# Kernel optimization log

Hardware: AMD Instinct MI355X
Metric: run time of the kernel (lower is better)

The kernel has to match this reference:

```python
import jax, jax.numpy as jnp
import numpy as np

D_MODEL = 1024
N_HEADS = 16
D_K = D_MODEL // N_HEADS
NEG_INF = -1.0e9


def setup_inputs() -> dict:
    key = jax.random.key(0)
    ks = jax.random.split(key, 12)
    B, S = 2, 2048
    inp = {
        "q": jax.random.normal(ks[0], (B, S, D_MODEL), dtype=jnp.float32),
        "k": jax.random.normal(ks[1], (B, S, D_MODEL), dtype=jnp.float32),
        "v": jax.random.normal(ks[2], (B, S, D_MODEL), dtype=jnp.float32),
        "mask": jax.random.randint(ks[3], (B, 1, S, S), 0, 2, dtype=jnp.int32),
        "Wq": jax.random.normal(ks[4], (D_MODEL, D_MODEL), dtype=jnp.float32) / np.sqrt(D_MODEL),
        "bq": jnp.zeros((D_MODEL,), dtype=jnp.float32),
        "Wk": jax.random.normal(ks[5], (D_MODEL, D_MODEL), dtype=jnp.float32) / np.sqrt(D_MODEL),
        "bk": jnp.zeros((D_MODEL,), dtype=jnp.float32),
        "Wv": jax.random.normal(ks[6], (D_MODEL, D_MODEL), dtype=jnp.float32) / np.sqrt(D_MODEL),
        "bv": jnp.zeros((D_MODEL,), dtype=jnp.float32),
        "Wo": jax.random.normal(ks[7], (D_MODEL, D_MODEL), dtype=jnp.float32) / np.sqrt(D_MODEL),
        "bo": jnp.zeros((D_MODEL,), dtype=jnp.float32),
    }
    return inp


def _split_heads(x):
    B, S, _ = x.shape
    return x.reshape(B, S, N_HEADS, D_K).transpose(0, 2, 1, 3)  # [B,H,S,Dk]


def reference(q, k, v, mask, Wq, bq, Wk, bk, Wv, bv, Wo, bo):
    # QKV projections (nn.Linear: x @ W.T + b; here W stored as [in,out]-agnostic square)
    query = _split_heads(q @ Wq + bq)
    key_ = _split_heads(k @ Wk + bk)
    value = _split_heads(v @ Wv + bv)

    scale = 1.0 / np.sqrt(D_K).astype(np.float32)
    scores = jnp.einsum("bhqd,bhkd->bhqk", query, key_) * scale  # [B,H,S,S]
    scores = jnp.where(mask == 0, NEG_INF, scores)
    attn = jax.nn.softmax(scores, axis=-1)  # dropout is identity in eval (p=0.0)
    ctx = jnp.einsum("bhqk,bhkd->bhqd", attn, value)  # [B,H,S,Dk]

    B, H, S, Dk = ctx.shape
    ctx = ctx.transpose(0, 2, 1, 3).reshape(B, S, H * Dk)
    return ctx @ Wo + bo
```

## Files before the change

### kernel.cpp

```cpp
#include <hip/hip_runtime.h>
#include <hip/hip_bf16.h>

typedef __bf16 bf16_t;
typedef __bf16 bf16x2 __attribute__((ext_vector_type(2)));
typedef __bf16 bf16x8 __attribute__((ext_vector_type(8)));
typedef float f32x4 __attribute__((ext_vector_type(4)));
typedef float f32x16 __attribute__((ext_vector_type(16)));
typedef unsigned int u32;
typedef unsigned long long u64;

#define S_LEN 2048
#define DM 1024
#define NH 16
#define DK 64
#define M_ROWS 4096
#define SCALE_LOG2E 0.1803368801111204f

__device__ __forceinline__ int sw_off(int row, int col) {
  return row * 64 + ((((col >> 3) ^ row) & 7) << 3) + (col & 7);
}

__device__ __forceinline__ bf16x8 cvt8(const float4& a, const float4& b) {
  bf16x8 v;
  v[0] = (__bf16)a.x; v[1] = (__bf16)a.y; v[2] = (__bf16)a.z; v[3] = (__bf16)a.w;
  v[4] = (__bf16)b.x; v[5] = (__bf16)b.y; v[6] = (__bf16)b.z; v[7] = (__bf16)b.w;
  return v;
}

__device__ __forceinline__ void glds16(const bf16_t* g, bf16_t* l) {
  __builtin_amdgcn_global_load_lds(
      (const __attribute__((address_space(1))) void*)g,
      (__attribute__((address_space(3))) void*)l, 16, 0, 0);
}

__device__ __forceinline__ u32 sbit(u32 m, int c) {
#if __has_builtin(__builtin_amdgcn_sbfe)
  return (u32)__builtin_amdgcn_sbfe((int)m, c, 1);
#else
  return (u32)(((int)(m << (31 - c))) >> 31);
#endif
}
__device__ __forceinline__ float mand(float p, u32 e) {
  return __builtin_bit_cast(float, __builtin_bit_cast(u32, p) & e);
}
__device__ __forceinline__ u32 pack2(float lo, float hi) {
#if __has_builtin(__builtin_amdgcn_cvt_pk_bf16_f32)
  bf16x2 r = __builtin_amdgcn_cvt_pk_bf16_f32(lo, hi);
  return __builtin_bit_cast(u32, r);
#else
  union { __bf16 h[2]; u32 u; } x;
  x.h[0] = (__bf16)lo; x.h[1] = (__bf16)hi;
  return x.u;
#endif
}

union U4B { uint4 u; bf16x8 v; };

__global__ __launch_bounds__(256) void pack_maskT(
    const int* __restrict__ mask, u64* __restrict__ mbT)
{
  const int g = blockIdx.x * 256 + threadIdx.x;
  const int key4 = (g & 511) * 4;
  const int qw = (g >> 9) & 31;
  const int b = g >> 14;
  const int* src = &mask[((size_t)b * S_LEN + qw * 64) * S_LEN + key4];
  u64 b0 = 0, b1 = 0, b2 = 0, b3 = 0;
  #pragma unroll 8
  for (int i = 0; i < 64; ++i) {
    const int4 v = *(const int4*)&src[(size_t)i * S_LEN];
    b0 |= (u64)(v.x != 0) << i;
    b1 |= (u64)(v.y != 0) << i;
    b2 |= (u64)(v.z != 0) << i;
    b3 |= (u64)(v.w != 0) << i;
  }
  u64* dst = &mbT[((size_t)b * 32 + qw) * S_LEN + key4];
  dst[0] = b0; dst[1] = b1; dst[2] = b2; dst[3] = b3;
}

__global__ __launch_bounds__(256) void cvt_inputs(
    const float* __restrict__ q, const float* __restrict__ k,
    const float* __restrict__ v, bf16_t* __restrict__ Xb)
{
  const int z = blockIdx.y;
  const float* __restrict__ src = (z == 0) ? q : ((z == 1) ? k : v);
  const size_t idx = ((size_t)blockIdx.x * 256 + threadIdx.x) * 8;
  const float4 a = *(const float4*)&src[idx];
  const float4 b = *(const float4*)&src[idx + 4];
  *(bf16x8*)&Xb[(size_t)z * M_ROWS * DM + idx] = cvt8(a, b);
}

__global__ __launch_bounds__(256) void transw_kernel(
    const float* __restrict__ Wq, const float* __restrict__ Wk,
    const float* __restrict__ Wv, const float* __restrict__ Wo,
    bf16_t* __restrict__ Wt)
{
  const int z = blockIdx.z;
  const float* __restrict__ W = (z == 0) ? Wq : ((z == 1) ? Wk : ((z == 2) ? Wv : Wo));
  bf16_t* __restrict__ out = Wt + (size_t)z * DM * DM;
  __shared__ float tile[64][65];
  const int tx = threadIdx.x & 31, ty = threadIdx.x >> 5;
  const int k0 = blockIdx.x * 64, n0 = blockIdx.y * 64;
  #pragma unroll
  for (int j = 0; j < 8; ++j) {
    const float2 v = *(const float2*)&W[(size_t)(k0 + ty + 8 * j) * DM + n0 + tx * 2];
    tile[ty + 8 * j][tx * 2] = v.x;
    tile[ty + 8 * j][tx * 2 + 1] = v.y;
  }
  __syncthreads();
  #pragma unroll
  for (int j = 0; j < 8; ++j) {
    const int a = ty + 8 * j;
    bf16x2 p;
    p[0] = (__bf16)tile[tx * 2][a];
    p[1] = (__bf16)tile[tx * 2 + 1][a];
    *(bf16x2*)&out[(size_t)(n0 + a) * DM + k0 + tx * 2] = p;
  }
}

__device__ __forceinline__ void gemm_core(
    const bf16_t* __restrict__ A, const bf16_t* __restrict__ Bt,
    f32x4 (&acc)[4][4])
{
  __shared__ __align__(16) bf16_t As[128 * 32];
  __shared__ __align__(16) bf16_t Bs[128 * 32];
  const int t = threadIdx.x, w = t >> 6, L = t & 63, quad = L >> 4, l16 = L & 15;
  const int m0 = blockIdx.x * 128, n0 = blockIdx.y * 128;
  const int mb = 64 * (w & 1), nb = 64 * (w >> 1);
  const int rowS = t >> 2, subS = (t & 3) * 8;

  for (int k0 = 0; k0 < DM; k0 += 32) {
    __syncthreads();
    glds16(&A[(size_t)(m0 + rowS) * DM + k0 + subS],       &As[t * 8]);
    glds16(&A[(size_t)(m0 + 64 + rowS) * DM + k0 + subS],  &As[2048 + t * 8]);
    glds16(&Bt[(size_t)(n0 + rowS) * DM + k0 + subS],      &Bs[t * 8]);
    glds16(&Bt[(size_t)(n0 + 64 + rowS) * DM + k0 + subS], &Bs[2048 + t * 8]);
    __syncthreads();
    bf16x8 af[4], bfr[4];
    #pragma unroll
    for (int mt = 0; mt < 4; ++mt)
      af[mt] = *(const bf16x8*)&As[(mb + 16 * mt + l16) * 32 + quad * 8];
    #pragma unroll
    for (int ct = 0; ct < 4; ++ct)
      bfr[ct] = *(const bf16x8*)&Bs[(nb + 16 * ct + l16) * 32 + quad * 8];
    #pragma unroll
    for (int mt = 0; mt < 4; ++mt)
      #pragma unroll
      for (int ct = 0; ct < 4; ++ct)
        acc[mt][ct] = __builtin_amdgcn_mfma_f32_16x16x32_bf16(af[mt], bfr[ct], acc[mt][ct], 0, 0, 0);
  }
}

__global__ __launch_bounds__(256) void gemm_qkv(
    const bf16_t* __restrict__ Xb, const bf16_t* __restrict__ Wt,
    const float* __restrict__ bq, const float* __restrict__ bk,
    const float* __restrict__ bv,
    bf16_t* __restrict__ Qp, bf16_t* __restrict__ Ksw, bf16_t* __restrict__ Vpl)
{
  const int z = blockIdx.z;
  const float* __restrict__ bias = (z == 0) ? bq : ((z == 1) ? bk : bv);
  f32x4 acc[4][4] = {};
  gemm_core(Xb + (size_t)z * M_ROWS * DM, Wt + (size_t)z * DM * DM, acc);

  const int t = threadIdx.x, w = t >> 6, L = t & 63, quad = L >> 4, l16 = L & 15;
  const int m0 = blockIdx.x * 128, n0 = blockIdx.y * 128;
  const int mb = 64 * (w & 1), nb = 64 * (w >> 1);
  #pragma unroll
  for (int mt = 0; mt < 4; ++mt)
    #pragma unroll
    for (int ct = 0; ct < 4; ++ct)
      #pragma unroll
      for (int r = 0; r < 4; ++r) {
        const int row = m0 + mb + 16 * mt + quad * 4 + r;
        const int n = n0 + nb + 16 * ct + l16;
        float val = acc[mt][ct][r] + bias[n];
        if (z == 0) {
          Qp[(size_t)row * DM + n] = (__bf16)(val * SCALE_LOG2E);
        } else if (z == 2) {
          Vpl[(size_t)row * DM + n] = (__bf16)val;
        } else {
          const int b_ = row >> 11, s = row & 2047, h = n >> 6, d = n & 63;
          const int bh = b_ * NH + h;
          Ksw[((size_t)bh * 32 + (s >> 6)) * 4096 + sw_off(s & 63, d)] = (__bf16)val;
        }
      }
}

__global__ __launch_bounds__(256) void transpV(
    const bf16_t* __restrict__ Vpl, bf16_t* __restrict__ Vt_sw)
{
  __shared__ bf16_t Tr[64 * 72];
  const int t = threadIdx.x;
  const int key0 = blockIdx.x * 64;
  const int bh = blockIdx.y, b = bh >> 4, h = bh & 15;
  const int r = t >> 2, c = (t & 3) * 16;
  const bf16_t* src = &Vpl[(size_t)(b * S_LEN + key0 + r) * DM + h * DK + c];
  const bf16x8 v0 = *(const bf16x8*)src;
  const bf16x8 v1 = *(const bf16x8*)(src + 8);
  #pragma unroll
  for (int j = 0; j < 8; ++j) {
    Tr[r * 72 + c + j] = v0[j];
    Tr[r * 72 + c + 8 + j] = v1[j];
  }
  __syncthreads();
  const int dv = t >> 2, kc = (t & 3) * 16;
  bf16_t ov[16];
  #pragma unroll
  for (int j = 0; j < 16; ++j) ov[j] = Tr[(kc + j) * 72 + dv];
  bf16_t* dst = &Vt_sw[((size_t)bh * 32 + blockIdx.x) * 4096];
  *(bf16x8*)&dst[sw_off(dv, kc)]     = *(bf16x8*)&ov[0];
  *(bf16x8*)&dst[sw_off(dv, kc + 8)] = *(bf16x8*)&ov[8];
}

__global__ __launch_bounds__(256, 2) void attn_kernel(
    const bf16_t* __restrict__ Qp, const bf16_t* __restrict__ Ksw,
    const bf16_t* __restrict__ Vt_sw, const u64* __restrict__ mbT,
    bf16_t* __restrict__ ctx)
{
  __shared__ __align__(16) bf16_t KV[4 * 4096];
  __shared__ __align__(16) u32 Pd[64 * 68];

  const int t = threadIdx.x;
  const int w = t >> 6, L = t & 63;
  const int wq = w & 1, wk = w >> 1;
  const int l31 = L & 31, h5 = L >> 5;
  const int q0 = blockIdx.x * 128;
  const int bh = blockIdx.y, b = bh >> 4, h = bh & 15;

  bf16_t* K0 = KV;            bf16_t* K1 = KV + 4096;
  bf16_t* V0 = KV + 8192;     bf16_t* V1 = KV + 12288;

  const bf16_t* KbaseG = Ksw + (size_t)bh * 32 * 4096;
  const bf16_t* VbaseG = Vt_sw + (size_t)bh * 32 * 4096;

  bf16x8 qf[2][4];
  #pragma unroll
  for (int mt = 0; mt < 2; ++mt) {
    const bf16_t* qr = &Qp[((size_t)(b * S_LEN) + q0 + 64 * wq + 32 * mt + l31) * DM + h * DK + 8 * h5];
    #pragma unroll
    for (int ks = 0; ks < 4; ++ks) qf[mt][ks] = *(const bf16x8*)&qr[16 * ks];
  }

  bf16x8 ones;
  #pragma unroll
  for (int j = 0; j < 8; ++j) ones[j] = (__bf16)1.0f;

  const int qw = 2 * blockIdx.x + wq;
  const size_t mrow = ((size_t)b * 32 + qw) * S_LEN;
  const u32 sel = (l31 & 1) ? 0x07060302u : 0x05040100u;

  f32x16 O[2][2] = {};
  f32x16 Lacc[2] = {};

  glds16(KbaseG + t * 8, K0 + t * 8);
  glds16(KbaseG + 2048 + t * 8, K0 + 2048 + t * 8);
  glds16(VbaseG + t * 8, V0 + t * 8);
  glds16(VbaseG + 2048 + t * 8, V0 + 2048 + t * 8);

  auto iter = [&](int kt, bf16_t* Kc, bf16_t* Vc, bf16_t* Kn, bf16_t* Vn) {
    __syncthreads();
    const u64 mq = mbT[mrow + (size_t)kt * 64 + 32 * wk + l31];
    if (kt + 1 < 32) {
      const bf16_t* kg = KbaseG + (size_t)(kt + 1) * 4096;
      const bf16_t* vg = VbaseG + (size_t)(kt + 1) * 4096;
      glds16(kg + t * 8, Kn + t * 8);
      glds16(kg + 2048 + t * 8, Kn + 2048 + t * 8);
      glds16(vg + t * 8, Vn + t * 8);
      glds16(vg + 2048 + t * 8, Vn + 2048 + t * 8);
    }

    f32x16 sv[2] = {};
    #pragma unroll
    for (int ks = 0; ks < 4; ++ks) {
      const int ch = ((2 * ks + h5) ^ l31) & 7;
      const bf16x8 kb = *(const bf16x8*)&Kc[(32 * wk + l31) * 64 + ch * 8];
      sv[0] = __builtin_amdgcn_mfma_f32_32x32x16_bf16(qf[0][ks], kb, sv[0], 0, 0, 0);
      sv[1] = __builtin_amdgcn_mfma_f32_32x32x16_bf16(qf[1][ks], kb, sv[1], 0, 0, 0);
    }

    const u32 mlo = (u32)mq, mhi = (u32)(mq >> 32);
    #pragma unroll
    for (int mt = 0; mt < 2; ++mt) {
      const u32 mm = mt ? mhi : mlo;
      #pragma unroll
      for (int rp = 0; rp < 16; rp += 2) {
        const int c = (rp & 3) + 8 * (rp >> 2) + 4 * h5;
        const int p = 32 * wq + 16 * mt + (c >> 1);
        const float p0 = mand(__builtin_exp2f(sv[mt][rp]),     sbit(mm, c));
        const float p1 = mand(__builtin_exp2f(sv[mt][rp + 1]), sbit(mm, c + 1));
        Pd[p * 68 + 32 * wk + l31] = pack2(p0, p1);
      }
    }

    #pragma unroll
    for (int ks = 0; ks < 2; ++ks) {
      bf16x8 pa[2];
      #pragma unroll
      for (int mt = 0; mt < 2; ++mt) {
        const int p = 32 * wq + 16 * mt + (l31 >> 1);
        const int off = p * 68 + 32 * wk + 16 * ks + 8 * h5;
        const uint4 lo = *(const uint4*)&Pd[off];
        const uint4 hi = *(const uint4*)&Pd[off + 4];
        U4B af;
        af.u.x = __builtin_amdgcn_perm(lo.y, lo.x, sel);
        af.u.y = __builtin_amdgcn_perm(lo.w, lo.z, sel);
        af.u.z = __builtin_amdgcn_perm(hi.y, hi.x, sel);
        af.u.w = __builtin_amdgcn_perm(hi.w, hi.z, sel);
        pa[mt] = af.v;
      }
      #pragma unroll
      for (int dvt = 0; dvt < 2; ++dvt) {
        const int ch = ((4 * wk + 2 * ks + h5) ^ l31) & 7;
        const bf16x8 vb = *(const bf16x8*)&Vc[(32 * dvt + l31) * 64 + ch * 8];
        O[0][dvt] = __builtin_amdgcn_mfma_f32_32x32x16_bf16(pa[0], vb, O[0][dvt], 0, 0, 0);
        O[1][dvt] = __builtin_amdgcn_mfma_f32_32x32x16_bf16(pa[1], vb, O[1][dvt], 0, 0, 0);
      }
      Lacc[0] = __builtin_amdgcn_mfma_f32_32x32x16_bf16(pa[0], ones, Lacc[0], 0, 0, 0);
      Lacc[1] = __builtin_amdgcn_mfma_f32_32x32x16_bf16(pa[1], ones, Lacc[1], 0, 0, 0);
    }
  };

  for (int kt = 0; kt < 32; kt += 2) {
    iter(kt,     K0, V0, K1, V1);
    iter(kt + 1, K1, V1, K0, V0);
  }

  __syncthreads();
  float* Osh = (float*)KV;
  float* Lsh = (float*)Pd;
  if (wk == 0) {
    #pragma unroll
    for (int mt = 0; mt < 2; ++mt)
      #pragma unroll
      for (int r = 0; r < 16; ++r) {
        const int ql = 64 * wq + 32 * mt + (r & 3) + 8 * (r >> 2) + 4 * h5;
        Osh[ql * 64 + l31]      = O[mt][0][r];
        Osh[ql * 64 + 32 + l31] = O[mt][1][r];
        if (l31 == 0) Lsh[ql] = Lacc[mt][r];
      }
  }
  __syncthreads();
  if (wk == 1) {
    #pragma unroll
    for (int mt = 0; mt < 2; ++mt)
      #pragma unroll
      for (int r = 0; r < 16; ++r) {
        const int ql = 64 * wq + 32 * mt + (r & 3) + 8 * (r >> 2) + 4 * h5;
        const float inv = 1.0f / (Lacc[mt][r] + Lsh[ql]);
        const size_t obase = ((size_t)(b * S_LEN) + q0 + ql) * DM + h * DK;
        ctx[obase + l31]      = (__bf16)((O[mt][0][r] + Osh[ql * 64 + l31]) * inv);
        ctx[obase + 32 + l31] = (__bf16)((O[mt][1][r] + Osh[ql * 64 + 32 + l31]) * inv);
      }
  }
}

__global__ __launch_bounds__(256) void gemm_out(
    const bf16_t* __restrict__ ctx, const bf16_t* __restrict__ Wto,
    const float* __restrict__ bo, float* __restrict__ out)
{
  f32x4 acc[4][4] = {};
  gemm_core(ctx, Wto, acc);
  const int t = threadIdx.x, w = t >> 6, L = t & 63, quad = L >> 4, l16 = L & 15;
  const int m0 = blockIdx.x * 128, n0 = blockIdx.y * 128;
  const int mb = 64 * (w & 1), nb = 64 * (w >> 1);
  #pragma unroll
  for (int mt = 0; mt < 4; ++mt)
    #pragma unroll
    for (int ct = 0; ct < 4; ++ct)
      #pragma unroll
      for (int r = 0; r < 4; ++r) {
        const int row = m0 + mb + 16 * mt + quad * 4 + r;
        const int n = n0 + nb + 16 * ct + l16;
        out[(size_t)row * DM + n] = acc[mt][ct][r] + bo[n];
      }
}

extern "C" void kernel_launch(void* const* d_in, const int* in_sizes, int n_in,
                              void* d_out, int out_size, void* d_ws, size_t ws_size,
                              hipStream_t stream) {
  const float* q  = (const float*)d_in[0];
  const float* k  = (const float*)d_in[1];
  const float* v  = (const float*)d_in[2];
  const int* mask = (const int*)d_in[3];
  const float* Wq = (const float*)d_in[4];
  const float* bq = (const float*)d_in[5];
  const float* Wk = (const float*)d_in[6];
  const float* bk = (const float*)d_in[7];
  const float* Wv = (const float*)d_in[8];
  const float* bv = (const float*)d_in[9];
  const float* Wo = (const float*)d_in[10];
  const float* bo = (const float*)d_in[11];
  float* out = (float*)d_out;

  const size_t SLICE = (size_t)M_ROWS * DM;
  bf16_t* ws_b = (bf16_t*)d_ws;
  bf16_t* Xb    = ws_b;
  bf16_t* Qp    = ws_b + 3 * SLICE;
  bf16_t* Ksw   = ws_b + 4 * SLICE;
  bf16_t* Vpl   = ws_b + 5 * SLICE;
  bf16_t* Wt    = ws_b + 6 * SLICE;
  u64* mbT      = (u64*)(ws_b + 7 * SLICE);
  bf16_t* Vt_sw = ws_b + 2 * SLICE;
  bf16_t* ctx   = ws_b;

  pack_maskT<<<dim3(128), dim3(256), 0, stream>>>(mask, mbT);
  cvt_inputs<<<dim3(2048, 3), dim3(256), 0, stream>>>(q, k, v, Xb);
  transw_kernel<<<dim3(16, 16, 4), dim3(256), 0, stream>>>(Wq, Wk, Wv, Wo, Wt);
  gemm_qkv<<<dim3(32, 8, 3), dim3(256), 0, stream>>>(Xb, Wt, bq, bk, bv, Qp, Ksw, Vpl);
  transpV<<<dim3(32, 32), dim3(256), 0, stream>>>(Vpl, Vt_sw);
  attn_kernel<<<dim3(16, 32), dim3(256), 0, stream>>>(Qp, Ksw, Vt_sw, mbT, ctx);
  gemm_out<<<dim3(32, 8), dim3(256), 0, stream>>>(ctx, Wt + (size_t)3 * DM * DM, bo, out);
}
```

Before: 303.3 us.

## Fuse prep kernels, ballot-pack mask, keep attention P in registers via swapped MFMA

```diff
diff --git a/kernel.cpp b/kernel.cpp
--- a/kernel.cpp
+++ b/kernel.cpp
@@ -34,11 +34,7 @@
 }
 
 __device__ __forceinline__ u32 sbit(u32 m, int c) {
-#if __has_builtin(__builtin_amdgcn_sbfe)
-  return (u32)__builtin_amdgcn_sbfe((int)m, c, 1);
-#else
   return (u32)(((int)(m << (31 - c))) >> 31);
-#endif
 }
 __device__ __forceinline__ float mand(float p, u32 e) {
   return __builtin_bit_cast(float, __builtin_bit_cast(u32, p) & e);
@@ -56,64 +52,62 @@
 
 union U4B { uint4 u; bf16x8 v; };
 
-__global__ __launch_bounds__(256) void pack_maskT(
-    const int* __restrict__ mask, u64* __restrict__ mbT)
-{
-  const int g = blockIdx.x * 256 + threadIdx.x;
-  const int key4 = (g & 511) * 4;
-  const int qw = (g >> 9) & 31;
-  const int b = g >> 14;
-  const int* src = &mask[((size_t)b * S_LEN + qw * 64) * S_LEN + key4];
-  u64 b0 = 0, b1 = 0, b2 = 0, b3 = 0;
-  #pragma unroll 8
-  for (int i = 0; i < 64; ++i) {
-    const int4 v = *(const int4*)&src[(size_t)i * S_LEN];
-    b0 |= (u64)(v.x != 0) << i;
-    b1 |= (u64)(v.y != 0) << i;
-    b2 |= (u64)(v.z != 0) << i;
-    b3 |= (u64)(v.w != 0) << i;
-  }
-  u64* dst = &mbT[((size_t)b * 32 + qw) * S_LEN + key4];
-  dst[0] = b0; dst[1] = b1; dst[2] = b2; dst[3] = b3;
-}
-
-__global__ __launch_bounds__(256) void cvt_inputs(
-    const float* __restrict__ q, const float* __restrict__ k,
-    const float* __restrict__ v, bf16_t* __restrict__ Xb)
-{
-  const int z = blockIdx.y;
-  const float* __restrict__ src = (z == 0) ? q : ((z == 1) ? k : v);
-  const size_t idx = ((size_t)blockIdx.x * 256 + threadIdx.x) * 8;
-  const float4 a = *(const float4*)&src[idx];
-  const float4 b = *(const float4*)&src[idx + 4];
-  *(bf16x8*)&Xb[(size_t)z * M_ROWS * DM + idx] = cvt8(a, b);
-}
-
-__global__ __launch_bounds__(256) void transw_kernel(
+#define PREP_PACK_BLOCKS 8192
+#define PREP_CVT_BLOCKS  6144
+#define PREP_TW_BLOCKS   1024
+
+__global__ __launch_bounds__(256) void prep_kernel(
+    const int* __restrict__ mask,
+    const float* __restrict__ q, const float* __restrict__ k, const float* __restrict__ v,
     const float* __restrict__ Wq, const float* __restrict__ Wk,
     const float* __restrict__ Wv, const float* __restrict__ Wo,
-    bf16_t* __restrict__ Wt)
-{
-  const int z = blockIdx.z;
-  const float* __restrict__ W = (z == 0) ? Wq : ((z == 1) ? Wk : ((z == 2) ? Wv : Wo));
-  bf16_t* __restrict__ out = Wt + (size_t)z * DM * DM;
+    u64* __restrict__ mrowT, bf16_t* __restrict__ Xb, bf16_t* __restrict__ Wt)
+{
   __shared__ float tile[64][65];
-  const int tx = threadIdx.x & 31, ty = threadIdx.x >> 5;
-  const int k0 = blockIdx.x * 64, n0 = blockIdx.y * 64;
-  #pragma unroll
-  for (int j = 0; j < 8; ++j) {
-    const float2 v = *(const float2*)&W[(size_t)(k0 + ty + 8 * j) * DM + n0 + tx * 2];
-    tile[ty + 8 * j][tx * 2] = v.x;
-    tile[ty + 8 * j][tx * 2 + 1] = v.y;
-  }
-  __syncthreads();
-  #pragma unroll
-  for (int j = 0; j < 8; ++j) {
-    const int a = ty + 8 * j;
-    bf16x2 p;
-    p[0] = (__bf16)tile[tx * 2][a];
-    p[1] = (__bf16)tile[tx * 2 + 1][a];
-    *(bf16x2*)&out[(size_t)(n0 + a) * DM + k0 + tx * 2] = p;
+  const int bx = blockIdx.x;
+  if (bx < PREP_PACK_BLOCKS) {
+    const int gw = (bx * 256 + threadIdx.x) >> 6;
+    const int lane = threadIdx.x & 63;
+    const int kw0 = (gw & 7) * 4;
+    const int qr = (gw >> 3) & 2047;
+    const int b = gw >> 14;
+    #pragma unroll
+    for (int j = 0; j < 4; ++j) {
+      const int kw = kw0 + j;
+      const int mv = mask[((size_t)b * S_LEN + qr) * S_LEN + kw * 64 + lane];
+      const u64 bits = __ballot(mv != 0);
+      if (lane == 0) mrowT[((size_t)b * 32 + kw) * S_LEN + qr] = bits;
+    }
+  } else if (bx < PREP_PACK_BLOCKS + PREP_CVT_BLOCKS) {
+    const int id = bx - PREP_PACK_BLOCKS;
+    const int z = id >> 11, blk = id & 2047;
+    const float* __restrict__ src = (z == 0) ? q : ((z == 1) ? k : v);
+    const size_t idx = ((size_t)blk * 256 + threadIdx.x) * 8;
+    const float4 a = *(const float4*)&src[idx];
+    const float4 b4 = *(const float4*)&src[idx + 4];
+    *(bf16x8*)&Xb[(size_t)z * M_ROWS * DM + idx] = cvt8(a, b4);
+  } else {
+    const int id = bx - (PREP_PACK_BLOCKS + PREP_CVT_BLOCKS);
+    const int z = id >> 8, rem = id & 255;
+    const float* __restrict__ W = (z == 0) ? Wq : ((z == 1) ? Wk : ((z == 2) ? Wv : Wo));
+    bf16_t* __restrict__ out = Wt + (size_t)z * DM * DM;
+    const int tx = threadIdx.x & 31, ty = threadIdx.x >> 5;
+    const int k0 = (rem >> 4) * 64, n0 = (rem & 15) * 64;
+    #pragma unroll
+    for (int j = 0; j < 8; ++j) {
+      const float2 vv = *(const float2*)&W[(size_t)(k0 + ty + 8 * j) * DM + n0 + tx * 2];
+      tile[ty + 8 * j][tx * 2] = vv.x;
+      tile[ty + 8 * j][tx * 2 + 1] = vv.y;
+    }
+    __syncthreads();
+    #pragma unroll
+    for (int j = 0; j < 8; ++j) {
+      const int a = ty + 8 * j;
+      bf16x2 p;
+      p[0] = (__bf16)tile[tx * 2][a];
+      p[1] = (__bf16)tile[tx * 2 + 1][a];
+      *(bf16x2*)&out[(size_t)(n0 + a) * DM + k0 + tx * 2] = p;
+    }
   }
 }
 
@@ -211,61 +205,57 @@
   *(bf16x8*)&dst[sw_off(dv, kc + 8)] = *(bf16x8*)&ov[8];
 }
 
-__global__ __launch_bounds__(256, 2) void attn_kernel(
+__global__ __launch_bounds__(128, 2) void attn_kernel(
     const bf16_t* __restrict__ Qp, const bf16_t* __restrict__ Ksw,
-    const bf16_t* __restrict__ Vt_sw, const u64* __restrict__ mbT,
+    const bf16_t* __restrict__ Vt_sw, const u64* __restrict__ mrowT,
     bf16_t* __restrict__ ctx)
 {
   __shared__ __align__(16) bf16_t KV[4 * 4096];
-  __shared__ __align__(16) u32 Pd[64 * 68];
 
   const int t = threadIdx.x;
-  const int w = t >> 6, L = t & 63;
-  const int wq = w & 1, wk = w >> 1;
+  const int wk = t >> 6, L = t & 63;
   const int l31 = L & 31, h5 = L >> 5;
-  const int q0 = blockIdx.x * 128;
+  const int q0 = blockIdx.x * 64;
   const int bh = blockIdx.y, b = bh >> 4, h = bh & 15;
 
-  bf16_t* K0 = KV;            bf16_t* K1 = KV + 4096;
-  bf16_t* V0 = KV + 8192;     bf16_t* V1 = KV + 12288;
+  bf16_t* K0 = KV;        bf16_t* K1 = KV + 4096;
+  bf16_t* V0 = KV + 8192; bf16_t* V1 = KV + 12288;
 
   const bf16_t* KbaseG = Ksw + (size_t)bh * 32 * 4096;
   const bf16_t* VbaseG = Vt_sw + (size_t)bh * 32 * 4096;
 
   bf16x8 qf[2][4];
   #pragma unroll
-  for (int mt = 0; mt < 2; ++mt) {
-    const bf16_t* qr = &Qp[((size_t)(b * S_LEN) + q0 + 64 * wq + 32 * mt + l31) * DM + h * DK + 8 * h5];
-    #pragma unroll
-    for (int ks = 0; ks < 4; ++ks) qf[mt][ks] = *(const bf16x8*)&qr[16 * ks];
-  }
-
-  bf16x8 ones;
-  #pragma unroll
-  for (int j = 0; j < 8; ++j) ones[j] = (__bf16)1.0f;
-
-  const int qw = 2 * blockIdx.x + wq;
-  const size_t mrow = ((size_t)b * 32 + qw) * S_LEN;
-  const u32 sel = (l31 & 1) ? 0x07060302u : 0x05040100u;
+  for (int qb = 0; qb < 2; ++qb) {
+    const bf16_t* qr = &Qp[((size_t)(b * S_LEN) + q0 + 32 * qb + l31) * DM + h * DK + 8 * h5];
+    #pragma unroll
+    for (int ks = 0; ks < 4; ++ks) qf[qb][ks] = *(const bf16x8*)&qr[16 * ks];
+  }
+
+  const u64* mbase = &mrowT[(size_t)b * 32 * S_LEN + q0 + l31];
 
   f32x16 O[2][2] = {};
-  f32x16 Lacc[2] = {};
-
-  glds16(KbaseG + t * 8, K0 + t * 8);
-  glds16(KbaseG + 2048 + t * 8, K0 + 2048 + t * 8);
-  glds16(VbaseG + t * 8, V0 + t * 8);
-  glds16(VbaseG + 2048 + t * 8, V0 + 2048 + t * 8);
+  float lacc[2] = {0.f, 0.f};
+
+  auto stage = [&](int kt, bf16_t* Kd, bf16_t* Vd) {
+    const bf16_t* kg = KbaseG + (size_t)kt * 4096;
+    const bf16_t* vg = VbaseG + (size_t)kt * 4096;
+    #pragma unroll
+    for (int i = 0; i < 4; ++i) glds16(kg + i * 1024 + t * 8, Kd + i * 1024 + t * 8);
+    #pragma unroll
+    for (int i = 0; i < 4; ++i) glds16(vg + i * 1024 + t * 8, Vd + i * 1024 + t * 8);
+  };
+
+  u64 mp0 = mbase[0], mp1 = mbase[32];
+  stage(0, K0, V0);
 
   auto iter = [&](int kt, bf16_t* Kc, bf16_t* Vc, bf16_t* Kn, bf16_t* Vn) {
     __syncthreads();
-    const u64 mq = mbT[mrow + (size_t)kt * 64 + 32 * wk + l31];
+    const u64 mq0 = mp0, mq1 = mp1;
     if (kt + 1 < 32) {
-      const bf16_t* kg = KbaseG + (size_t)(kt + 1) * 4096;
-      const bf16_t* vg = VbaseG + (size_t)(kt + 1) * 4096;
-      glds16(kg + t * 8, Kn + t * 8);
-      glds16(kg + 2048 + t * 8, Kn + 2048 + t * 8);
-      glds16(vg + t * 8, Vn + t * 8);
-      glds16(vg + 2048 + t * 8, Vn + 2048 + t * 8);
+      mp0 = mbase[(size_t)(kt + 1) * S_LEN];
+      mp1 = mbase[(size_t)(kt + 1) * S_LEN + 32];
+      stage(kt + 1, Kn, Vn);
     }
 
     f32x16 sv[2] = {};
@@ -273,49 +263,55 @@
     for (int ks = 0; ks < 4; ++ks) {
       const int ch = ((2 * ks + h5) ^ l31) & 7;
       const bf16x8 kb = *(const bf16x8*)&Kc[(32 * wk + l31) * 64 + ch * 8];
-      sv[0] = __builtin_amdgcn_mfma_f32_32x32x16_bf16(qf[0][ks], kb, sv[0], 0, 0, 0);
-      sv[1] = __builtin_amdgcn_mfma_f32_32x32x16_bf16(qf[1][ks], kb, sv[1], 0, 0, 0);
-    }
-
-    const u32 mlo = (u32)mq, mhi = (u32)(mq >> 32);
-    #pragma unroll
-    for (int mt = 0; mt < 2; ++mt) {
-      const u32 mm = mt ? mhi : mlo;
-      #pragma unroll
-      for (int rp = 0; rp < 16; rp += 2) {
-        const int c = (rp & 3) + 8 * (rp >> 2) + 4 * h5;
-        const int p = 32 * wq + 16 * mt + (c >> 1);
-        const float p0 = mand(__builtin_exp2f(sv[mt][rp]),     sbit(mm, c));
-        const float p1 = mand(__builtin_exp2f(sv[mt][rp + 1]), sbit(mm, c + 1));
-        Pd[p * 68 + 32 * wk + l31] = pack2(p0, p1);
+      sv[0] = __builtin_amdgcn_mfma_f32_32x32x16_bf16(kb, qf[0][ks], sv[0], 0, 0, 0);
+      sv[1] = __builtin_amdgcn_mfma_f32_32x32x16_bf16(kb, qf[1][ks], sv[1], 0, 0, 0);
+    }
+
+    u32 fr[2][2][4];
+    #pragma unroll
+    for (int qb = 0; qb < 2; ++qb) {
+      const u32 mh = (u32)((qb ? mq1 : mq0) >> (32 * wk));
+      float p[16];
+      #pragma unroll
+      for (int r = 0; r < 16; ++r) {
+        const int bit = (r & 3) + 8 * (r >> 2) + 4 * h5;
+        p[r] = mand(__builtin_exp2f(sv[qb][r]), sbit(mh, bit));
       }
+      lacc[qb] += ((p[0] + p[1]) + (p[2] + p[3])) + ((p[4] + p[5]) + (p[6] + p[7]))
+                + ((p[8] + p[9]) + (p[10] + p[11])) + ((p[12] + p[13]) + (p[14] + p[15]));
+      u32 D[8];
+      #pragma unroll
+      for (int j = 0; j < 8; ++j) D[j] = pack2(p[2 * j], p[2 * j + 1]);
+      const u32 S0 = h5 ? D[0] : D[2];
+      const u32 S1 = h5 ? D[1] : D[3];
+      const u32 S2 = h5 ? D[4] : D[6];
+      const u32 S3 = h5 ? D[5] : D[7];
+      const u32 R0 = (u32)__shfl_xor((int)S0, 32);
+      const u32 R1 = (u32)__shfl_xor((int)S1, 32);
+      const u32 R2 = (u32)__shfl_xor((int)S2, 32);
+      const u32 R3 = (u32)__shfl_xor((int)S3, 32);
+      fr[qb][0][0] = h5 ? R0 : D[0];
+      fr[qb][0][1] = h5 ? R1 : D[1];
+      fr[qb][0][2] = h5 ? D[2] : R0;
+      fr[qb][0][3] = h5 ? D[3] : R1;
+      fr[qb][1][0] = h5 ? R2 : D[4];
+      fr[qb][1][1] = h5 ? R3 : D[5];
+      fr[qb][1][2] = h5 ? D[6] : R2;
+      fr[qb][1][3] = h5 ? D[7] : R3;
     }
 
     #pragma unroll
     for (int ks = 0; ks < 2; ++ks) {
-      bf16x8 pa[2];
-      #pragma unroll
-      for (int mt = 0; mt < 2; ++mt) {
-        const int p = 32 * wq + 16 * mt + (l31 >> 1);
-        const int off = p * 68 + 32 * wk + 16 * ks + 8 * h5;
-        const uint4 lo = *(const uint4*)&Pd[off];
-        const uint4 hi = *(const uint4*)&Pd[off + 4];
-        U4B af;
-        af.u.x = __builtin_amdgcn_perm(lo.y, lo.x, sel);
-        af.u.y = __builtin_amdgcn_perm(lo.w, lo.z, sel);
-        af.u.z = __builtin_amdgcn_perm(hi.y, hi.x, sel);
-        af.u.w = __builtin_amdgcn_perm(hi.w, hi.z, sel);
-        pa[mt] = af.v;
+      U4B pf0, pf1;
+      pf0.u = *(uint4*)fr[0][ks];
+      pf1.u = *(uint4*)fr[1][ks];
+      #pragma unroll
+      for (int dvb = 0; dvb < 2; ++dvb) {
+        const int ch = ((4 * wk + 2 * ks + h5) ^ l31) & 7;
+        const bf16x8 vb = *(const bf16x8*)&Vc[(32 * dvb + l31) * 64 + ch * 8];
+        O[0][dvb] = __builtin_amdgcn_mfma_f32_32x32x16_bf16(vb, pf0.v, O[0][dvb], 0, 0, 0);
+        O[1][dvb] = __builtin_amdgcn_mfma_f32_32x32x16_bf16(vb, pf1.v, O[1][dvb], 0, 0, 0);
       }
-      #pragma unroll
-      for (int dvt = 0; dvt < 2; ++dvt) {
-        const int ch = ((4 * wk + 2 * ks + h5) ^ l31) & 7;
-        const bf16x8 vb = *(const bf16x8*)&Vc[(32 * dvt + l31) * 64 + ch * 8];
-        O[0][dvt] = __builtin_amdgcn_mfma_f32_32x32x16_bf16(pa[0], vb, O[0][dvt], 0, 0, 0);
-        O[1][dvt] = __builtin_amdgcn_mfma_f32_32x32x16_bf16(pa[1], vb, O[1][dvt], 0, 0, 0);
-      }
-      Lacc[0] = __builtin_amdgcn_mfma_f32_32x32x16_bf16(pa[0], ones, Lacc[0], 0, 0, 0);
-      Lacc[1] = __builtin_amdgcn_mfma_f32_32x32x16_bf16(pa[1], ones, Lacc[1], 0, 0, 0);
     }
   };
 
@@ -325,31 +321,54 @@
   }
 
   __syncthreads();
-  float* Osh = (float*)KV;
-  float* Lsh = (float*)Pd;
+  u32* OshU = (u32*)KV;
+  float* Lsh = (float*)(OshU + 64 * 36);
   if (wk == 0) {
     #pragma unroll
-    for (int mt = 0; mt < 2; ++mt)
-      #pragma unroll
-      for (int r = 0; r < 16; ++r) {
-        const int ql = 64 * wq + 32 * mt + (r & 3) + 8 * (r >> 2) + 4 * h5;
-        Osh[ql * 64 + l31]      = O[mt][0][r];
-        Osh[ql * 64 + 32 + l31] = O[mt][1][r];
-        if (l31 == 0) Lsh[ql] = Lacc[mt][r];
-      }
+    for (int qb = 0; qb < 2; ++qb) {
+      const float ls = lacc[qb] + __shfl_xor(lacc[qb], 32);
+      if (h5 == 0) Lsh[32 * qb + l31] = ls;
+      #pragma unroll
+      for (int dvb = 0; dvb < 2; ++dvb)
+        #pragma unroll
+        for (int r = 0; r < 16; r += 2) {
+          const int col = 16 * dvb + ((r & 3) >> 1) + 4 * (r >> 2) + 2 * h5;
+          OshU[(32 * qb + l31) * 36 + col] = pack2(O[qb][dvb][r], O[qb][dvb][r + 1]);
+        }
+    }
   }
   __syncthreads();
   if (wk == 1) {
     #pragma unroll
-    for (int mt = 0; mt < 2; ++mt)
-      #pragma unroll
-      for (int r = 0; r < 16; ++r) {
-        const int ql = 64 * wq + 32 * mt + (r & 3) + 8 * (r >> 2) + 4 * h5;
-        const float inv = 1.0f / (Lacc[mt][r] + Lsh[ql]);
-        const size_t obase = ((size_t)(b * S_LEN) + q0 + ql) * DM + h * DK;
-        ctx[obase + l31]      = (__bf16)((O[mt][0][r] + Osh[ql * 64 + l31]) * inv);
-        ctx[obase + 32 + l31] = (__bf16)((O[mt][1][r] + Osh[ql * 64 + 32 + l31]) * inv);
-      }
+    for (int qb = 0; qb < 2; ++qb) {
+      const float ls = lacc[qb] + __shfl_xor(lacc[qb], 32) + Lsh[32 * qb + l31];
+      const float inv = 1.0f / ls;
+      #pragma unroll
+      for (int dvb = 0; dvb < 2; ++dvb)
+        #pragma unroll
+        for (int r = 0; r < 16; r += 2) {
+          const int col = 16 * dvb + ((r & 3) >> 1) + 4 * (r >> 2) + 2 * h5;
+          const u32 d = OshU[(32 * qb + l31) * 36 + col];
+          const float a0 = __builtin_bit_cast(float, d << 16);
+          const float a1 = __builtin_bit_cast(float, d & 0xffff0000u);
+          OshU[(32 * qb + l31) * 36 + col] =
+              pack2((a0 + O[qb][dvb][r]) * inv, (a1 + O[qb][dvb][r + 1]) * inv);
+        }
+    }
+  }
+  __syncthreads();
+  {
+    const int qr = t >> 1, half = t & 1;
+    const u32* src = &OshU[qr * 36 + 16 * half];
+    const uint4 x0 = *(const uint4*)&src[0];
+    const uint4 x1 = *(const uint4*)&src[4];
+    const uint4 x2 = *(const uint4*)&src[8];
+    const uint4 x3 = *(const uint4*)&src[12];
+    bf16_t* dst = &ctx[((size_t)(b * S_LEN) + q0 + qr) * DM + h * DK + 32 * half];
+    *(uint4*)&dst[0]  = x0;
+    *(uint4*)&dst[8]  = x1;
+    *(uint4*)&dst[16] = x2;
+    *(uint4*)&dst[24] = x3;
   }
 }
 
@@ -398,15 +417,14 @@
   bf16_t* Ksw   = ws_b + 4 * SLICE;
   bf16_t* Vpl   = ws_b + 5 * SLICE;
   bf16_t* Wt    = ws_b + 6 * SLICE;
-  u64* mbT      = (u64*)(ws_b + 7 * SLICE);
+  u64* mrowT    = (u64*)(ws_b + 7 * SLICE);
   bf16_t* Vt_sw = ws_b + 2 * SLICE;
   bf16_t* ctx   = ws_b;
 
-  pack_maskT<<<dim3(128), dim3(256), 0, stream>>>(mask, mbT);
-  cvt_inputs<<<dim3(2048, 3), dim3(256), 0, stream>>>(q, k, v, Xb);
-  transw_kernel<<<dim3(16, 16, 4), dim3(256), 0, stream>>>(Wq, Wk, Wv, Wo, Wt);
+  prep_kernel<<<dim3(PREP_PACK_BLOCKS + PREP_CVT_BLOCKS + PREP_TW_BLOCKS),
+                dim3(256), 0, stream>>>(mask, q, k, v, Wq, Wk, Wv, Wo, mrowT, Xb, Wt);
   gemm_qkv<<<dim3(32, 8, 3), dim3(256), 0, stream>>>(Xb, Wt, bq, bk, bv, Qp, Ksw, Vpl);
   transpV<<<dim3(32, 32), dim3(256), 0, stream>>>(Vpl, Vt_sw);
-  attn_kernel<<<dim3(16, 32), dim3(256), 0, stream>>>(Qp, Ksw, Vt_sw, mbT, ctx);
+  attn_kernel<<<dim3(32, 32), dim3(128), 0, stream>>>(Qp, Ksw, Vt_sw, mrowT, ctx);
   gemm_out<<<dim3(32, 8), dim3(256), 0, stream>>>(ctx, Wt + (size_t)3 * DM * DM, bo, out);
 }
```

Measured after the change: 293.7 us. -3.2%, faster.
